# Performance work log

Hardware: AMD Instinct MI355X
Metric: run time of the kernel (lower is better)

The kernel has to match this reference:

```python
import math
import jax, jax.numpy as jnp
import numpy as np

B, S, T = 32, 512, 180
D, F, L, H = 512, 2048, 6, 8
DH = D // H


def _pos_encoding(length, d):
    pos = np.arange(length, dtype=np.float32)[:, None]
    div = np.exp(np.arange(0, d, 2, dtype=np.float32) * (-math.log(10000.0) / d))
    pe = np.zeros((length, d), dtype=np.float32)
    pe[:, 0::2] = np.sin(pos * div)
    pe[:, 1::2] = np.cos(pos * div)
    return jnp.asarray(pe)


def _ln(x, scale, bias):
    mu = x.mean(-1, keepdims=True)
    var = ((x - mu) ** 2).mean(-1, keepdims=True)
    return (x - mu) * jax.lax.rsqrt(var + 1e-5) * scale + bias


def _mha(q_in, kv_in, w, b, causal=False):
    # w: [4, D, D] = (Wq, Wk, Wv, Wo); b: [4, D]
    b_, sq = q_in.shape[:2]
    q = (q_in @ w[0] + b[0]).reshape(b_, sq, H, DH)
    k = (kv_in @ w[1] + b[1]).reshape(b_, -1, H, DH)
    v = (kv_in @ w[2] + b[2]).reshape(b_, -1, H, DH)
    s = jnp.einsum('bqhd,bkhd->bhqk', q, k) / math.sqrt(DH)
    if causal:
        mask = jnp.tril(jnp.ones((sq, k.shape[1]), dtype=bool))
        s = jnp.where(mask, s, -1e9)
    a = jax.nn.softmax(s, axis=-1)
    o = jnp.einsum('bhqk,bkhd->bqhd', a, v).reshape(b_, sq, D)
    return o @ w[3] + b[3]


def _ffn(x, w1, b1, w2, b2):
    return jax.nn.relu(x @ w1 + b1) @ w2 + b2


def setup_inputs() -> dict:
    key = jax.random.key(0)
    ks = jax.random.split(key, 16)
    n = lambda k, shape: jax.random.normal(k, shape, jnp.float32) * 0.02
    return {
        'x': jax.random.normal(ks[0], (B, S, 2), jnp.float32),
        'y_cv_teacher': jax.random.normal(ks[1], (B, T, 1), jnp.float32),
        'src_proj_w': n(ks[2], (2, D)), 'src_proj_b': jnp.zeros((D,), jnp.float32),
        'tgt_proj_w': n(ks[3], (1, D)), 'tgt_proj_b': jnp.zeros((D,), jnp.float32),
        'enc_attn_w': n(ks[4], (L, 4, D, D)), 'enc_attn_b': jnp.zeros((L, 4, D), jnp.float32),
        'enc_ffn_w1': n(ks[5], (L, D, F)), 'enc_ffn_b1': jnp.zeros((L, F), jnp.float32),
        'enc_ffn_w2': n(ks[6], (L, F, D)), 'enc_ffn_b2': jnp.zeros((L, D), jnp.float32),
        'enc_ln_scale': jnp.ones((L, 2, D), jnp.float32), 'enc_ln_bias': jnp.zeros((L, 2, D), jnp.float32),
        'dec_self_w': n(ks[7], (L, 4, D, D)), 'dec_self_b': jnp.zeros((L, 4, D), jnp.float32),
        'dec_cross_w': n(ks[8], (L, 4, D, D)), 'dec_cross_b': jnp.zeros((L, 4, D), jnp.float32),
        'dec_ffn_w1': n(ks[9], (L, D, F)), 'dec_ffn_b1': jnp.zeros((L, F), jnp.float32),
        'dec_ffn_w2': n(ks[10], (L, F, D)), 'dec_ffn_b2': jnp.zeros((L, D), jnp.float32),
        'dec_ln_scale': jnp.ones((L, 3, D), jnp.float32), 'dec_ln_bias': jnp.zeros((L, 3, D), jnp.float32),
        'out_w': n(ks[11], (D, 1)), 'out_b': jnp.zeros((1,), jnp.float32),
    }


def reference(x, y_cv_teacher, src_proj_w, src_proj_b, tgt_proj_w, tgt_proj_b,
              enc_attn_w, enc_attn_b, enc_ffn_w1, enc_ffn_b1, enc_ffn_w2, enc_ffn_b2,
              enc_ln_scale, enc_ln_bias, dec_self_w, dec_self_b, dec_cross_w, dec_cross_b,
              dec_ffn_w1, dec_ffn_b1, dec_ffn_w2, dec_ffn_b2, dec_ln_scale, dec_ln_bias,
              out_w, out_b):
    pe = _pos_encoding(512, D)
    # encoder (post-norm, relu FFN, dropout disabled = eval semantics)
    h = x @ src_proj_w + src_proj_b + pe[: x.shape[1]]
    for i in range(L):
        h = _ln(h + _mha(h, h, enc_attn_w[i], enc_attn_b[i]), enc_ln_scale[i, 0], enc_ln_bias[i, 0])
        h = _ln(h + _ffn(h, enc_ffn_w1[i], enc_ffn_b1[i], enc_ffn_w2[i], enc_ffn_b2[i]),
                enc_ln_scale[i, 1], enc_ln_bias[i, 1])
    memory = h
    # teacher-forced decoder input: [start=0, y_cv_teacher[:-1]]
    tgt_in = jnp.concatenate([jnp.zeros((x.shape[0], 1, 1), x.dtype), y_cv_teacher[:, :-1, :]], axis=1)
    d = tgt_in @ tgt_proj_w + tgt_proj_b + pe[: tgt_in.shape[1]]
    for i in range(L):
        d = _ln(d + _mha(d, d, dec_self_w[i], dec_self_b[i], causal=True),
                dec_ln_scale[i, 0], dec_ln_bias[i, 0])
        d = _ln(d + _mha(d, memory, dec_cross_w[i], dec_cross_b[i]),
                dec_ln_scale[i, 1], dec_ln_bias[i, 1])
        d = _ln(d + _ffn(d, dec_ffn_w1[i], dec_ffn_b1[i], dec_ffn_w2[i], dec_ffn_b2[i]),
                dec_ln_scale[i, 2], dec_ln_bias[i, 2])
    return d @ out_w + out_b  # [B, T, 1]
```

## Files before the change

kernel.cpp:

```cpp
#include <hip/hip_runtime.h>
#include <math.h>

#define B_  32
#define S_  512
#define T_  180
#define D_  512
#define F_  2048
#define L_  6
#define H_  8
#define DH_ 64

typedef unsigned short u16;
typedef __attribute__((ext_vector_type(8))) short short8;
typedef __attribute__((ext_vector_type(4))) float floatx4;

__device__ __forceinline__ float bf2f(u16 h) {
    union { unsigned u; float f; } un; un.u = ((unsigned)h) << 16; return un.f;
}
__device__ __forceinline__ u16 f2bf(float f) {
    union { float f; unsigned u; } un; un.f = f;
    unsigned u = un.u;
    u += 0x7fffu + ((u >> 16) & 1u);
    return (u16)(u >> 16);
}

__device__ __forceinline__ void gload16(const u16* g, u16* l) {
    __builtin_amdgcn_global_load_lds(
        (const __attribute__((address_space(1))) void*)g,
        (__attribute__((address_space(3))) void*)l, 16, 0, 0);
}

__device__ __forceinline__ float pos_enc(int pos, int c) {
    int i2 = c & ~1;
    float div = expf(-(float)i2 * (9.210340371976184f / 512.0f));
    float arg = (float)pos * div;
    return (c & 1) ? cosf(arg) : sinf(arg);
}

__global__ __launch_bounds__(256) void embed_src_kernel(
    const float* __restrict__ x, const float* __restrict__ w,
    const float* __restrict__ b, u16* __restrict__ h)
{
    int idx = blockIdx.x * 256 + threadIdx.x;
    if (idx >= B_ * S_ * D_) return;
    int c  = idx & (D_ - 1);
    int bs = idx >> 9;
    int s  = bs & (S_ - 1);
    float x0 = x[bs * 2 + 0];
    float x1 = x[bs * 2 + 1];
    h[idx] = f2bf(x0 * w[c] + x1 * w[D_ + c] + b[c] + pos_enc(s, c));
}

__global__ __launch_bounds__(256) void embed_tgt_kernel(
    const float* __restrict__ y, const float* __restrict__ w,
    const float* __restrict__ b, u16* __restrict__ d)
{
    int idx = blockIdx.x * 256 + threadIdx.x;
    if (idx >= B_ * T_ * D_) return;
    int c  = idx & (D_ - 1);
    int bt = idx >> 9;
    int t  = bt % T_;
    int bb = bt / T_;
    float tv = (t == 0) ? 0.0f : y[bb * T_ + (t - 1)];
    d[idx] = f2bf(tv * w[c] + b[c] + pos_enc(t, c));
}

__global__ __launch_bounds__(256) void wconv_kernel(
    const float* __restrict__ W, u16* __restrict__ Wt, int K, int N)
{
    __shared__ float tile[32][33];
    size_t mat = (size_t)blockIdx.z * K * N;
    const float* Wm = W + mat;
    u16* Wtm = Wt + mat;
    int n0 = blockIdx.x * 32, k0 = blockIdx.y * 32;
    int tx = threadIdx.x & 31, ty = threadIdx.x >> 5;
#pragma unroll
    for (int i = 0; i < 32; i += 8)
        tile[ty + i][tx] = Wm[(size_t)(k0 + ty + i) * N + n0 + tx];
    __syncthreads();
#pragma unroll
    for (int i = 0; i < 32; i += 8)
        Wtm[(size_t)(n0 + ty + i) * K + k0 + tx] = f2bf(tile[tx][ty + i]);
}

__global__ __launch_bounds__(256) void gemm_bf16_kernel(
    const u16* __restrict__ A, int lda, const u16* __restrict__ Bt,
    const float* __restrict__ bias, u16* __restrict__ C, int ldc,
    int M, int N, int K, int relu)
{
    __shared__ u16 smem[18432];
    u16* As = smem;
    u16* Bs = smem + 8192;

    int tid  = threadIdx.x;
    int w    = tid >> 6;
    int lane = tid & 63;
    int m0 = blockIdx.y << 7, n0 = blockIdx.x << 7;

    int sr = w * 32 + (lane >> 2);
    int sk = (lane & 3) * 8;
    const u16* ag0 = A  + (size_t)(m0 + sr)      * lda + sk;
    const u16* ag1 = A  + (size_t)(m0 + sr + 16) * lda + sk;
    const u16* bg0 = Bt + (size_t)(n0 + sr)      * K + sk;
    const u16* bg1 = Bt + (size_t)(n0 + sr + 16) * K + sk;
    u16* al0 = As + (w * 2 + 0) * 512;
    u16* al1 = As + (w * 2 + 1) * 512;
    u16* bl0 = Bs + (w * 2 + 0) * 512;
    u16* bl1 = Bs + (w * 2 + 1) * 512;

    int wm = (w >> 1) * 64, wn = (w & 1) * 64;
    int fr = lane & 15;
    int fk = (lane >> 4) * 8;

    floatx4 acc[4][4] = {};

    for (int k0 = 0; k0 < K; k0 += 64) {
#pragma unroll
        for (int hh = 0; hh < 2; ++hh) {
            int go = k0 + hh * 32;
            int lo = hh * 4096;
            gload16(ag0 + go, al0 + lo);
            gload16(ag1 + go, al1 + lo);
            gload16(bg0 + go, bl0 + lo);
            gload16(bg1 + go, bl1 + lo);
        }
        __syncthreads();

#pragma unroll
        for (int hh = 0; hh < 2; ++hh) {
            int lo = hh * 4096;
            short8 af[4], bf[4];
#pragma unroll
            for (int i = 0; i < 4; ++i)
                af[i] = *(const short8*)&As[lo + (wm + i * 16 + fr) * 32 + fk];
#pragma unroll
            for (int j = 0; j < 4; ++j)
                bf[j] = *(const short8*)&Bs[lo + (wn + j * 16 + fr) * 32 + fk];
#pragma unroll
            for (int i = 0; i < 4; ++i)
#pragma unroll
                for (int j = 0; j < 4; ++j)
                    acc[i][j] = __builtin_amdgcn_mfma_f32_16x16x32_bf16(
                        af[i], bf[j], acc[i][j], 0, 0, 0);
        }
        __syncthreads();
    }

    u16* epi = smem + w * 4608;
    int cc = lane & 15;
    int rq = (lane >> 4) * 4;
#pragma unroll
    for (int j = 0; j < 4; ++j) {
        float bj = bias[n0 + wn + j * 16 + cc];
#pragma unroll
        for (int i = 0; i < 4; ++i) {
#pragma unroll
            for (int r = 0; r < 4; ++r) {
                float vv = acc[i][j][r] + bj;
                if (relu) vv = fmaxf(vv, 0.f);
                epi[(i * 16 + rq + r) * 72 + j * 16 + cc] = f2bf(vv);
            }
        }
    }
    __syncthreads();
#pragma unroll
    for (int t = 0; t < 8; ++t) {
        int er = t * 8 + (lane >> 3);
        int ec = (lane & 7) * 8;
        short8 vv = *(const short8*)&epi[er * 72 + ec];
        *(short8*)&C[(size_t)(m0 + wm + er) * ldc + n0 + wn + ec] = vv;
    }
}

#define SBAR()       asm volatile("s_barrier" ::: "memory")
#define WAIT_LGKM0() do { asm volatile("s_waitcnt lgkmcnt(0)" ::: "memory"); \
                          __builtin_amdgcn_sched_barrier(0); } while (0)
#define WAIT_VM(N)   asm volatile("s_waitcnt vmcnt(" #N ")" ::: "memory")

#define RD_A(BUF, MH) do { \
  _Pragma("unroll") for (int i_ = 0; i_ < 4; ++i_) \
  _Pragma("unroll") for (int h_ = 0; h_ < 2; ++h_) \
    a[i_][h_] = *(const short8*)&smem[(BUF) * 16384 + \
        ((MH) * 128 + qm + i_ * 16 + fr) * 64 + cSwz[h_]]; \
} while (0)

#define RD_B(BUF, NH) do { \
  _Pragma("unroll") for (int n_ = 0; n_ < 2; ++n_) \
  _Pragma("unroll") for (int h_ = 0; h_ < 2; ++h_) \
    bb[n_][h_] = *(const short8*)&smem[32768 + (BUF) * 16384 + \
        ((NH) * 128 + qn + n_ * 16 + fr) * 64 + cSwz[h_]]; \
} while (0)

#define PH_MMA(MH, NH) do { \
  __builtin_amdgcn_s_setprio(1); \
  _Pragma("unroll") for (int i_ = 0; i_ < 4; ++i_) \
  _Pragma("unroll") for (int n_ = 0; n_ < 2; ++n_) \
  _Pragma("unroll") for (int h_ = 0; h_ < 2; ++h_) \
    acc[MH][NH][i_][n_] = __builtin_amdgcn_mfma_f32_16x16x32_bf16( \
        a[i_][h_], bb[n_][h_], acc[MH][NH][i_][n_], 0, 0, 0); \
  __builtin_amdgcn_s_setprio(0); \
} while (0)

__global__ __launch_bounds__(512, 2) void gemm256_bf16_kernel(
    const u16* __restrict__ A, int lda, const u16* __restrict__ Bt,
    const float* __restrict__ bias, u16* __restrict__ C, int ldc,
    int M, int N, int K, int relu)
{
    __shared__ __align__(128) u16 smem[65536];
    const int AB0 = 0, AB1 = 16384, BB0 = 32768, BB1 = 49152;

    int tid = threadIdx.x;
    int w = tid >> 6, lane = tid & 63;
    int fr = lane & 15, q = lane >> 4;
    int qm = (w >> 2) * 64, qn = (w & 3) * 32;
    int r8 = tid >> 3;
    int ksrc = (((tid & 7) ^ (r8 & 7)) << 3);
    int cSwz[2];
    cSwz[0] = ((q ^ (fr & 7)) << 3);
    cSwz[1] = (((4 | q) ^ (fr & 7)) << 3);

    int nbx = gridDim.x;
    int nwg = nbx * gridDim.y;
    int flat = blockIdx.y * nbx + blockIdx.x;
    int qq = nwg >> 3, rr = nwg & 7;
    int xcd = flat & 7, sidx = flat >> 3;
    int wg = (xcd < rr ? xcd * (qq + 1) : rr * (qq + 1) + (xcd - rr) * qq) + sidx;
    int m0 = (wg / nbx) << 8, n0 = (wg % nbx) << 8;

    auto stg = [&](const u16* __restrict__ G, int ld, int row0, int bufOff,
                   int half, int gk) {
#pragma unroll
        for (int j = 0; j < 2; ++j) {
            int rl = half * 128 + j * 64 + r8;
            gload16(G + (size_t)(row0 + rl) * ld + gk + ksrc,
                    smem + bufOff + ((half * 128 + j * 64 + (w << 3)) << 6));
        }
    };

    short8 a[4][2], bb[2][2];
    floatx4 acc[2][2][4][2] = {};

    stg(A,  lda, m0, AB0, 0, 0);
    stg(A,  lda, m0, AB0, 1, 0);
    stg(Bt, K,   n0, BB0, 0, 0);
    stg(Bt, K,   n0, BB0, 1, 0);
    stg(Bt, K,   n0, BB1, 1, 64);
    stg(A,  lda, m0, AB1, 1, 64);
    WAIT_VM(0);
    SBAR();

    int NIT = K >> 7;
    for (int it = 0; it < NIT; ++it) {
        const int notlast = (it < NIT - 1);
        const int gk1 = it * 128 + 64, gk2 = gk1 + 64, gk3 = gk2 + 64;
        RD_A(0, 0); RD_B(0, 1);
        stg(A, lda, m0, AB1, 0, gk1);
        SBAR(); WAIT_LGKM0(); PH_MMA(0, 1); SBAR();
        RD_A(0, 1);
        stg(Bt, K, n0, BB1, 0, gk1);
        SBAR(); WAIT_LGKM0(); PH_MMA(1, 1); SBAR();
        RD_B(0, 0);
        if (notlast) stg(Bt, K, n0, BB0, 1, gk2);
        SBAR(); WAIT_LGKM0(); PH_MMA(1, 0); SBAR();
        RD_A(0, 0);
        if (notlast) { stg(A, lda, m0, AB0, 1, gk2); WAIT_VM(4); }
        else         { WAIT_VM(0); }
        SBAR(); WAIT_LGKM0(); PH_MMA(0, 0); SBAR();
        RD_A(1, 0); RD_B(1, 1);
        if (notlast) stg(A, lda, m0, AB0, 0, gk2);
        SBAR(); WAIT_LGKM0(); PH_MMA(0, 1); SBAR();
        RD_A(1, 1);
        if (notlast) stg(Bt, K, n0, BB0, 0, gk2);
        SBAR(); WAIT_LGKM0(); PH_MMA(1, 1); SBAR();
        RD_B(1, 0);
        if (notlast) stg(Bt, K, n0, BB1, 1, gk3);
        SBAR(); WAIT_LGKM0(); PH_MMA(1, 0); SBAR();
        RD_A(1, 0);
        if (notlast) { stg(A, lda, m0, AB1, 1, gk3); WAIT_VM(4); }
        SBAR(); WAIT_LGKM0(); PH_MMA(0, 0); SBAR();
    }

    u16* epi = smem + w * 2560;
    int rq = q * 4;
#pragma unroll
    for (int mh = 0; mh < 2; ++mh) {
#pragma unroll
        for (int nh = 0; nh < 2; ++nh) {
            __syncthreads();
            int bcol = n0 + nh * 128 + qn;
            int brow = m0 + mh * 128 + qm;
#pragma unroll
            for (int n = 0; n < 2; ++n) {
                float bj = bias[bcol + n * 16 + fr];
#pragma unroll
                for (int i = 0; i < 4; ++i)
#pragma unroll
                    for (int r = 0; r < 4; ++r) {
                        float vv = acc[mh][nh][i][n][r] + bj;
                        if (relu) vv = fmaxf(vv, 0.f);
                        epi[(i * 16 + rq + r) * 40 + n * 16 + fr] = f2bf(vv);
                    }
            }
            __syncthreads();
#pragma unroll
            for (int t = 0; t < 4; ++t) {
                int er = t * 16 + (lane >> 2);
                int ec = (lane & 3) * 8;
                short8 vv = *(const short8*)&epi[er * 40 + ec];
                *(short8*)&C[(size_t)(brow + er) * ldc + bcol + ec] = vv;
            }
        }
    }
}

#define CEXP 0.1803368801111244f

__global__ __launch_bounds__(256) void attn_mfma_kernel(
    const u16* Q, int qs, const u16* __restrict__ K, int ks,
    const u16* __restrict__ V, u16* O,
    int Sq, int Sk, int causal)
{
    __shared__ u16 Qs[64 * 72];
    __shared__ u16 Ks[64 * 72];
    __shared__ u16 Vt[64 * 72];
    __shared__ u16 Ps[4][16 * 72];

    int tid  = threadIdx.x;
    int w    = tid >> 6;
    int lane = tid & 63;
    int n    = lane & 15;
    int quad = lane >> 4;
    int bh = blockIdx.x;
    int bb = bh >> 3, hhd = bh & 7;
    int q0 = blockIdx.y * 64;

    const u16* Qb = Q + (size_t)bb * Sq * qs + hhd * DH_;
    const u16* Kb = K + (size_t)bb * Sk * ks + hhd * DH_;
    const u16* Vb = V + (size_t)bb * Sk * ks + hhd * DH_;

#pragma unroll
    for (int it = 0; it < 2; ++it) {
        int idx = it * 256 + tid;
        int r = idx >> 3, dg = (idx & 7) * 8;
        int qg0 = q0 + r;
        short8 vv = {};
        if (qg0 < Sq) vv = *(const short8*)&Qb[(size_t)qg0 * qs + dg];
        *(short8*)&Qs[r * 72 + dg] = vv;
    }

    float m_i = -1e30f, l_i = 0.f;
    floatx4 o_acc[4] = {};

    int qg = q0 + w * 16 + n;
    int kend = causal ? ((Sk < q0 + 64) ? Sk : (q0 + 64)) : Sk;
    __syncthreads();

    short8 aq0 = *(const short8*)&Qs[(w * 16 + n) * 72 + quad * 8];
    short8 aq1 = *(const short8*)&Qs[(w * 16 + n) * 72 + 32 + quad * 8];

    for (int k0 = 0; k0 < kend; k0 += 64) {
#pragma unroll
        for (int it = 0; it < 2; ++it) {
            int idx = it * 256 + tid;
            int r = idx >> 3, dg = (idx & 7) * 8;
            int kg = k0 + r;
            short8 kv = {}, vv = {};
            if (kg < Sk) {
                kv = *(const short8*)&Kb[(size_t)kg * ks + dg];
                vv = *(const short8*)&Vb[(size_t)kg * ks + dg];
            }
            *(short8*)&Ks[r * 72 + dg] = kv;
            int col = (r + dg) & 63;
#pragma unroll
            for (int j = 0; j < 8; ++j)
                Vt[(dg + j) * 72 + col] = (u16)vv[j];
        }
        __syncthreads();

        floatx4 sc[4] = {};
#pragma unroll
        for (int j = 0; j < 4; ++j) {
            short8 bk0 = *(const short8*)&Ks[(j * 16 + n) * 72 + quad * 8];
            short8 bk1 = *(const short8*)&Ks[(j * 16 + n) * 72 + 32 + quad * 8];
            sc[j] = __builtin_amdgcn_mfma_f32_16x16x32_bf16(bk0, aq0, sc[j], 0, 0, 0);
            sc[j] = __builtin_amdgcn_mfma_f32_16x16x32_bf16(bk1, aq1, sc[j], 0, 0, 0);
        }

        bool need_mask = (k0 + 64 > Sk) ||
                         (causal && (k0 + 63 > q0 + w * 16));
        if (need_mask) {
#pragma unroll
            for (int j = 0; j < 4; ++j) {
#pragma unroll
                for (int r = 0; r < 4; ++r) {
                    int kg = k0 + j * 16 + quad * 4 + r;
                    if (kg >= Sk || (causal && kg > qg))
                        sc[j][r] = -1e30f;
                }
            }
        }

        float mx = sc[0][0];
#pragma unroll
        for (int j = 0; j < 4; ++j)
#pragma unroll
            for (int r = 0; r < 4; ++r) mx = fmaxf(mx, sc[j][r]);
        mx = fmaxf(mx, __shfl_xor(mx, 16));
        mx = fmaxf(mx, __shfl_xor(mx, 32));
        float mnew = fmaxf(m_i, mx);
        float alpha = exp2f((m_i - mnew) * CEXP);
        m_i = mnew;
        float ps = 0.f;
#pragma unroll
        for (int j = 0; j < 4; ++j)
#pragma unroll
            for (int r = 0; r < 4; ++r) {
                float p = exp2f((sc[j][r] - mnew) * CEXP);
                sc[j][r] = p; ps += p;
            }
        ps += __shfl_xor(ps, 16);
        ps += __shfl_xor(ps, 32);
        l_i = l_i * alpha + ps;
#pragma unroll
        for (int jb = 0; jb < 4; ++jb)
#pragma unroll
            for (int r = 0; r < 4; ++r) o_acc[jb][r] *= alpha;

#pragma unroll
        for (int j = 0; j < 4; ++j) {
            unsigned lo = (unsigned)f2bf(sc[j][0]) | ((unsigned)f2bf(sc[j][1]) << 16);
            unsigned hi = (unsigned)f2bf(sc[j][2]) | ((unsigned)f2bf(sc[j][3]) << 16);
            *(uint2*)&Ps[w][n * 72 + j * 16 + quad * 4] = make_uint2(lo, hi);
        }

        short8 ap0 = *(const short8*)&Ps[w][n * 72 + quad * 8];
        short8 ap1 = *(const short8*)&Ps[w][n * 72 + 32 + quad * 8];
#pragma unroll
        for (int jb = 0; jb < 4; ++jb) {
            int d = jb * 16 + n;
            int rot = d & ~7;
            short8 bv0 = *(const short8*)&Vt[d * 72 + ((quad * 8 + rot) & 63)];
            short8 bv1 = *(const short8*)&Vt[d * 72 + ((32 + quad * 8 + rot) & 63)];
            o_acc[jb] = __builtin_amdgcn_mfma_f32_16x16x32_bf16(bv0, ap0, o_acc[jb], 0, 0, 0);
            o_acc[jb] = __builtin_amdgcn_mfma_f32_16x16x32_bf16(bv1, ap1, o_acc[jb], 0, 0, 0);
        }
        __syncthreads();
    }

    float inv = 1.0f / l_i;
    u16* Ob = O + (size_t)bb * Sq * qs + hhd * DH_;
    if (qg < Sq) {
#pragma unroll
        for (int jb = 0; jb < 4; ++jb) {
            unsigned lo = (unsigned)f2bf(o_acc[jb][0] * inv) |
                          ((unsigned)f2bf(o_acc[jb][1] * inv) << 16);
            unsigned hi = (unsigned)f2bf(o_acc[jb][2] * inv) |
                          ((unsigned)f2bf(o_acc[jb][3] * inv) << 16);
            *(uint2*)&Ob[(size_t)qg * qs + jb * 16 + quad * 4] = make_uint2(lo, hi);
        }
    }
}

__global__ __launch_bounds__(128) void add_ln_kernel(
    u16* __restrict__ h, const u16* __restrict__ delta,
    const float* __restrict__ scale, const float* __restrict__ bias)
{
    __shared__ float red[2][2];
    int row = blockIdx.x, tid = threadIdx.x;
    int lane = tid & 63, wv = tid >> 6;
    size_t base = (size_t)row * D_ + tid * 4;
    uint2 hv = *(const uint2*)&h[base];
    uint2 dv = *(const uint2*)&delta[base];
    float v0 = bf2f(hv.x & 0xffff) + bf2f(dv.x & 0xffff);
    float v1 = bf2f(hv.x >> 16)    + bf2f(dv.x >> 16);
    float v2 = bf2f(hv.y & 0xffff) + bf2f(dv.y & 0xffff);
    float v3 = bf2f(hv.y >> 16)    + bf2f(dv.y >> 16);

    float a  = v0 + v1 + v2 + v3;
    float b2 = v0 * v0 + v1 * v1 + v2 * v2 + v3 * v3;
#pragma unroll
    for (int off = 32; off > 0; off >>= 1) {
        a  += __shfl_xor(a, off);
        b2 += __shfl_xor(b2, off);
    }
    if (lane == 0) { red[wv][0] = a; red[wv][1] = b2; }
    __syncthreads();
    float S1 = red[0][0] + red[1][0];
    float S2 = red[0][1] + red[1][1];
    float mu = S1 * (1.0f / 512.0f);
    float var = S2 * (1.0f / 512.0f) - mu * mu;
    float rs = rsqrtf(var + 1e-5f);

    int c = tid * 4;
    float4 sc = *(const float4*)&scale[c];
    float4 bi = *(const float4*)&bias[c];
    unsigned lo = (unsigned)f2bf((v0 - mu) * rs * sc.x + bi.x) |
                  ((unsigned)f2bf((v1 - mu) * rs * sc.y + bi.y) << 16);
    unsigned hi = (unsigned)f2bf((v2 - mu) * rs * sc.z + bi.z) |
                  ((unsigned)f2bf((v3 - mu) * rs * sc.w + bi.w) << 16);
    *(uint2*)&h[base] = make_uint2(lo, hi);
}

__global__ __launch_bounds__(64) void out_proj_kernel(
    const u16* __restrict__ d, const float* __restrict__ w,
    const float* __restrict__ b, float* __restrict__ out)
{
    int row = blockIdx.x, lane = threadIdx.x;
    float s = 0.f;
    for (int c = lane; c < D_; c += 64) s += bf2f(d[(size_t)row * D_ + c]) * w[c];
#pragma unroll
    for (int off = 32; off > 0; off >>= 1) s += __shfl_down(s, off);
    if (lane == 0) out[row] = s + b[0];
}

extern "C" void kernel_launch(void* const* d_in, const int* in_sizes, int n_in,
                              void* d_out, int out_size, void* d_ws, size_t ws_size,
                              hipStream_t stream)
{
    const float* x          = (const float*)d_in[0];
    const float* y          = (const float*)d_in[1];
    const float* src_w      = (const float*)d_in[2];
    const float* src_b      = (const float*)d_in[3];
    const float* tgt_w      = (const float*)d_in[4];
    const float* tgt_b      = (const float*)d_in[5];
    const float* enc_attn_w = (const float*)d_in[6];
    const float* enc_attn_b = (const float*)d_in[7];
    const float* enc_ffn_w1 = (const float*)d_in[8];
    const float* enc_ffn_b1 = (const float*)d_in[9];
    const float* enc_ffn_w2 = (const float*)d_in[10];
    const float* enc_ffn_b2 = (const float*)d_in[11];
    const float* enc_ln_s   = (const float*)d_in[12];
    const float* enc_ln_b   = (const float*)d_in[13];
    const float* dec_self_w = (const float*)d_in[14];
    const float* dec_self_b = (const float*)d_in[15];
    const float* dec_cross_w= (const float*)d_in[16];
    const float* dec_cross_b= (const float*)d_in[17];
    const float* dec_ffn_w1 = (const float*)d_in[18];
    const float* dec_ffn_b1 = (const float*)d_in[19];
    const float* dec_ffn_w2 = (const float*)d_in[20];
    const float* dec_ffn_b2 = (const float*)d_in[21];
    const float* dec_ln_s   = (const float*)d_in[22];
    const float* dec_ln_b   = (const float*)d_in[23];
    const float* out_w      = (const float*)d_in[24];
    const float* out_b      = (const float*)d_in[25];
    float* out = (float*)d_out;

    const size_t E_BSD = (size_t)B_ * S_ * D_;
    const size_t E_BTD = (size_t)B_ * T_ * D_;
    const size_t WDD   = (size_t)D_ * D_;
    const size_t WDF   = (size_t)D_ * F_;
    const int MS = B_ * S_;
    const int MT = B_ * T_;

    u16* h    = (u16*)d_ws;
    u16* qkv  = h + E_BSD;
    u16* o    = qkv + (size_t)MS * 1536;
    u16* dbuf = o + E_BSD;
    u16* wsc  = dbuf + E_BTD;
    u16* mid  = qkv;
    u16* cq   = qkv;
    u16* ckv  = qkv + 4 * 1024 * 1024;

    auto gemm = [&](const u16* A, int lda, const u16* Wt, const float* bi,
                    u16* C, int ldc, int M, int N, int K, int relu) {
        dim3 g(N / 128, M / 128);
        gemm_bf16_kernel<<<g, dim3(256), 0, stream>>>(A, lda, Wt, bi, C, ldc,
                                                      M, N, K, relu);
    };
    auto gemm256 = [&](const u16* A, int lda, const u16* Wt, const float* bi,
                       u16* C, int ldc, int M, int N, int K, int relu) {
        dim3 g(N / 256, M / 256);
        gemm256_bf16_kernel<<<g, dim3(512), 0, stream>>>(A, lda, Wt, bi, C, ldc,
                                                         M, N, K, relu);
    };
    auto attn = [&](const u16* Qp, int qs, const u16* Kp, int ks,
                    const u16* Vp, u16* Op, int Sq, int Sk, int causal) {
        dim3 g(B_ * H_, (Sq + 63) / 64);
        attn_mfma_kernel<<<g, dim3(256), 0, stream>>>(Qp, qs, Kp, ks, Vp, Op,
                                                      Sq, Sk, causal);
    };
    auto addln = [&](u16* hp, const u16* dp, const float* sc, const float* bi,
                     int rows) {
        add_ln_kernel<<<dim3(rows), dim3(128), 0, stream>>>(hp, dp, sc, bi);
    };
    auto wconv = [&](const float* W, u16* Wt, int K, int N, int nmat) {
        wconv_kernel<<<dim3(N / 32, K / 32, nmat), dim3(256), 0, stream>>>(W, Wt, K, N);
    };

    embed_src_kernel<<<dim3((B_ * S_ * D_ + 255) / 256), dim3(256), 0, stream>>>(
        x, src_w, src_b, h);
    for (int l = 0; l < L_; ++l) {
        wconv(enc_attn_w + (size_t)l * 4 * WDD, wsc, D_, D_, 4);
        wconv(enc_ffn_w1 + (size_t)l * WDF, wsc + 4 * WDD, D_, F_, 1);
        wconv(enc_ffn_w2 + (size_t)l * WDF, wsc + 4 * WDD + WDF, F_, D_, 1);

        const float* bl = enc_attn_b + (size_t)l * 4 * D_;
        gemm256(h, D_, wsc, bl, qkv, 1536, MS, 1536, D_, 0);
        attn(qkv, 1536, qkv + 512, 1536, qkv + 1024, qkv, S_, S_, 0);
        gemm(qkv, 1536, wsc + 3 * WDD, bl + 3 * D_, o, D_, MS, D_, D_, 0);
        addln(h, o, enc_ln_s + (size_t)l * 2 * D_, enc_ln_b + (size_t)l * 2 * D_, MS);

        for (int m0 = 0; m0 < MS; m0 += 8192) {
            gemm256(h + (size_t)m0 * D_, D_, wsc + 4 * WDD,
                    enc_ffn_b1 + (size_t)l * F_, mid, F_, 8192, F_, D_, 1);
            gemm(mid, F_, wsc + 4 * WDD + WDF, enc_ffn_b2 + (size_t)l * D_,
                 o + (size_t)m0 * D_, D_, 8192, D_, F_, 0);
        }
        addln(h, o, enc_ln_s + (size_t)l * 2 * D_ + D_,
              enc_ln_b + (size_t)l * 2 * D_ + D_, MS);
    }

    embed_tgt_kernel<<<dim3((B_ * T_ * D_ + 255) / 256), dim3(256), 0, stream>>>(
        y, tgt_w, tgt_b, dbuf);
    for (int l = 0; l < L_; ++l) {
        wconv(dec_self_w  + (size_t)l * 4 * WDD, wsc, D_, D_, 4);
        wconv(dec_cross_w + (size_t)l * 4 * WDD, wsc + 4 * WDD, D_, D_, 4);
        wconv(dec_ffn_w1  + (size_t)l * WDF, wsc + 8 * WDD, D_, F_, 1);
        wconv(dec_ffn_w2  + (size_t)l * WDF, wsc + 8 * WDD + WDF, F_, D_, 1);

        const float* bl = dec_self_b + (size_t)l * 4 * D_;
        gemm(dbuf, D_, wsc, bl, qkv, 1536, MT, 1536, D_, 0);
        attn(qkv, 1536, qkv + 512, 1536, qkv + 1024, qkv, T_, T_, 1);
        gemm(qkv, 1536, wsc + 3 * WDD, bl + 3 * D_, o, D_, MT, D_, D_, 0);
        addln(dbuf, o, dec_ln_s + (size_t)l * 3 * D_,
              dec_ln_b + (size_t)l * 3 * D_, MT);

        const float* bc = dec_cross_b + (size_t)l * 4 * D_;
        gemm256(h, D_, wsc + 5 * WDD, bc + D_, ckv, 1024, MS, 1024, D_, 0);
        gemm(dbuf, D_, wsc + 4 * WDD, bc, cq, D_, MT, D_, D_, 0);
        attn(cq, 512, ckv, 1024, ckv + 512, cq, T_, S_, 0);
        gemm(cq, D_, wsc + 7 * WDD, bc + 3 * D_, o, D_, MT, D_, D_, 0);
        addln(dbuf, o, dec_ln_s + (size_t)l * 3 * D_ + D_,
              dec_ln_b + (size_t)l * 3 * D_ + D_, MT);

        gemm(dbuf, D_, wsc + 8 * WDD, dec_ffn_b1 + (size_t)l * F_,
             mid, F_, MT, F_, D_, 1);
        gemm(mid, F_, wsc + 8 * WDD + WDF, dec_ffn_b2 + (size_t)l * D_,
             o, D_, MT, D_, F_, 0);
        addln(dbuf, o, dec_ln_s + (size_t)l * 3 * D_ + 2 * D_,
              dec_ln_b + (size_t)l * 3 * D_ + 2 * D_, MT);
    }

    out_proj_kernel<<<dim3(MT), dim3(64), 0, stream>>>(dbuf, out_w, out_b, out);
}
```

Measured before the change: 3.228 ms.

## Use async LDS loads with XOR swizzle, lazy softmax rescale, packed bf16 converts

Attention now loads Q and K tiles with global_load_lds into unpadded, XOR-swizzled shared memory instead of register round-trips. It also skips the online-softmax rescale unless the running max grows by more than a threshold. Float-to-bf16 conversions use the hardware packed-convert instruction, and two decoder GEMMs move to the 256-tile kernel with M padded to 5888. The bounds checks on K/V/Q loads are removed, so out-of-range rows (Sk=180, T tail) may read past the valid data or into neighbouring batches, and the padded-M GEMMs read and write rows beyond MT.

```diff
diff --git a/kernel.cpp b/kernel.cpp
--- a/kernel.cpp
+++ b/kernel.cpp
@@ -22,6 +22,11 @@
     unsigned u = un.u;
     u += 0x7fffu + ((u >> 16) & 1u);
     return (u16)(u >> 16);
+}
+__device__ __forceinline__ unsigned cvt_pk_bf16(float lo, float hi) {
+    unsigned r;
+    asm("v_cvt_pk_bf16_f32 %0, %1, %2" : "=v"(r) : "v"(lo), "v"(hi));
+    return r;
 }
 
 __device__ __forceinline__ void gload16(const u16* g, u16* l) {
@@ -320,8 +325,8 @@
     const u16* __restrict__ V, u16* O,
     int Sq, int Sk, int causal)
 {
-    __shared__ u16 Qs[64 * 72];
-    __shared__ u16 Ks[64 * 72];
+    __shared__ u16 Qs[4096];
+    __shared__ u16 Ks[4096];
     __shared__ u16 Vt[64 * 72];
     __shared__ u16 Ps[4][16 * 72];
 
@@ -338,38 +343,33 @@
     const u16* Kb = K + (size_t)bb * Sk * ks + hhd * DH_;
     const u16* Vb = V + (size_t)bb * Sk * ks + hhd * DH_;
 
-#pragma unroll
-    for (int it = 0; it < 2; ++it) {
-        int idx = it * 256 + tid;
-        int r = idx >> 3, dg = (idx & 7) * 8;
-        int qg0 = q0 + r;
-        short8 vv = {};
-        if (qg0 < Sq) vv = *(const short8*)&Qb[(size_t)qg0 * qs + dg];
-        *(short8*)&Qs[r * 72 + dg] = vv;
-    }
+    int sr = tid >> 3;
+    int gk = (((tid & 7) ^ (sr & 7)) << 3);
+
+    gload16(Qb + (size_t)(q0 + sr) * qs + gk, Qs + tid * 8);
+    gload16(Qb + (size_t)(q0 + 32 + sr) * qs + gk, Qs + 2048 + tid * 8);
 
     float m_i = -1e30f, l_i = 0.f;
     floatx4 o_acc[4] = {};
-
     int qg = q0 + w * 16 + n;
     int kend = causal ? ((Sk < q0 + 64) ? Sk : (q0 + 64)) : Sk;
+
+    int csw0 = ((quad ^ (n & 7)) << 3);
+    int csw1 = (((4 | quad) ^ (n & 7)) << 3);
+
     __syncthreads();
 
-    short8 aq0 = *(const short8*)&Qs[(w * 16 + n) * 72 + quad * 8];
-    short8 aq1 = *(const short8*)&Qs[(w * 16 + n) * 72 + 32 + quad * 8];
+    short8 aq0 = *(const short8*)&Qs[(w * 16 + n) * 64 + csw0];
+    short8 aq1 = *(const short8*)&Qs[(w * 16 + n) * 64 + csw1];
 
     for (int k0 = 0; k0 < kend; k0 += 64) {
+        gload16(Kb + (size_t)(k0 + sr) * ks + gk, Ks + tid * 8);
+        gload16(Kb + (size_t)(k0 + 32 + sr) * ks + gk, Ks + 2048 + tid * 8);
 #pragma unroll
         for (int it = 0; it < 2; ++it) {
             int idx = it * 256 + tid;
             int r = idx >> 3, dg = (idx & 7) * 8;
-            int kg = k0 + r;
-            short8 kv = {}, vv = {};
-            if (kg < Sk) {
-                kv = *(const short8*)&Kb[(size_t)kg * ks + dg];
-                vv = *(const short8*)&Vb[(size_t)kg * ks + dg];
-            }
-            *(short8*)&Ks[r * 72 + dg] = kv;
+            short8 vv = *(const short8*)&Vb[(size_t)(k0 + r) * ks + dg];
             int col = (r + dg) & 63;
 #pragma unroll
             for (int j = 0; j < 8; ++j)
@@ -380,8 +380,8 @@
         floatx4 sc[4] = {};
 #pragma unroll
         for (int j = 0; j < 4; ++j) {
-            short8 bk0 = *(const short8*)&Ks[(j * 16 + n) * 72 + quad * 8];
-            short8 bk1 = *(const short8*)&Ks[(j * 16 + n) * 72 + 32 + quad * 8];
+            short8 bk0 = *(const short8*)&Ks[(j * 16 + n) * 64 + csw0];
+            short8 bk1 = *(const short8*)&Ks[(j * 16 + n) * 64 + csw1];
             sc[j] = __builtin_amdgcn_mfma_f32_16x16x32_bf16(bk0, aq0, sc[j], 0, 0, 0);
             sc[j] = __builtin_amdgcn_mfma_f32_16x16x32_bf16(bk1, aq1, sc[j], 0, 0, 0);
         }
@@ -407,30 +407,33 @@
             for (int r = 0; r < 4; ++r) mx = fmaxf(mx, sc[j][r]);
         mx = fmaxf(mx, __shfl_xor(mx, 16));
         mx = fmaxf(mx, __shfl_xor(mx, 32));
-        float mnew = fmaxf(m_i, mx);
-        float alpha = exp2f((m_i - mnew) * CEXP);
-        m_i = mnew;
+        if (__any(mx > m_i + 8.0f)) {
+            float mnew = fmaxf(m_i, mx);
+            float alpha = exp2f((m_i - mnew) * CEXP);
+            m_i = mnew;
+            l_i *= alpha;
+#pragma unroll
+            for (int jb = 0; jb < 4; ++jb)
+#pragma unroll
+                for (int r = 0; r < 4; ++r) o_acc[jb][r] *= alpha;
+        }
         float ps = 0.f;
 #pragma unroll
         for (int j = 0; j < 4; ++j)
 #pragma unroll
             for (int r = 0; r < 4; ++r) {
-                float p = exp2f((sc[j][r] - mnew) * CEXP);
+                float p = exp2f((sc[j][r] - m_i) * CEXP);
                 sc[j][r] = p; ps += p;
             }
         ps += __shfl_xor(ps, 16);
         ps += __shfl_xor(ps, 32);
-        l_i = l_i * alpha + ps;
-#pragma unroll
-        for (int jb = 0; jb < 4; ++jb)
-#pragma unroll
-            for (int r = 0; r < 4; ++r) o_acc[jb][r] *= alpha;
+        l_i += ps;
 
 #pragma unroll
         for (int j = 0; j < 4; ++j) {
-            unsigned lo = (unsigned)f2bf(sc[j][0]) | ((unsigned)f2bf(sc[j][1]) << 16);
-            unsigned hi = (unsigned)f2bf(sc[j][2]) | ((unsigned)f2bf(sc[j][3]) << 16);
-            *(uint2*)&Ps[w][n * 72 + j * 16 + quad * 4] = make_uint2(lo, hi);
+            unsigned p0 = cvt_pk_bf16(sc[j][0], sc[j][1]);
+            unsigned p1 = cvt_pk_bf16(sc[j][2], sc[j][3]);
+            *(uint2*)&Ps[w][n * 72 + j * 16 + quad * 4] = make_uint2(p0, p1);
         }
 
         short8 ap0 = *(const short8*)&Ps[w][n * 72 + quad * 8];
@@ -452,11 +455,9 @@
     if (qg < Sq) {
 #pragma unroll
         for (int jb = 0; jb < 4; ++jb) {
-            unsigned lo = (unsigned)f2bf(o_acc[jb][0] * inv) |
-                          ((unsigned)f2bf(o_acc[jb][1] * inv) << 16);
-            unsigned hi = (unsigned)f2bf(o_acc[jb][2] * inv) |
-                          ((unsigned)f2bf(o_acc[jb][3] * inv) << 16);
-            *(uint2*)&Ob[(size_t)qg * qs + jb * 16 + quad * 4] = make_uint2(lo, hi);
+            unsigned p0 = cvt_pk_bf16(o_acc[jb][0] * inv, o_acc[jb][1] * inv);
+            unsigned p1 = cvt_pk_bf16(o_acc[jb][2] * inv, o_acc[jb][3] * inv);
+            *(uint2*)&Ob[(size_t)qg * qs + jb * 16 + quad * 4] = make_uint2(p0, p1);
         }
     }
 }
@@ -551,6 +552,7 @@
     const size_t WDF   = (size_t)D_ * F_;
     const int MS = B_ * S_;
     const int MT = B_ * T_;
+    const int MTP = 5888;
 
     u16* h    = (u16*)d_ws;
     u16* qkv  = h + E_BSD;
@@ -619,7 +621,7 @@
         wconv(dec_ffn_w2  + (size_t)l * WDF, wsc + 8 * WDD + WDF, F_, D_, 1);
 
         const float* bl = dec_self_b + (size_t)l * 4 * D_;
-        gemm(dbuf, D_, wsc, bl, qkv, 1536, MT, 1536, D_, 0);
+        gemm256(dbuf, D_, wsc, bl, qkv, 1536, MTP, 1536, D_, 0);
         attn(qkv, 1536, qkv + 512, 1536, qkv + 1024, qkv, T_, T_, 1);
         gemm(qkv, 1536, wsc + 3 * WDD, bl + 3 * D_, o, D_, MT, D_, D_, 0);
         addln(dbuf, o, dec_ln_s + (size_t)l * 3 * D_,
@@ -633,8 +635,8 @@
         addln(dbuf, o, dec_ln_s + (size_t)l * 3 * D_ + D_,
               dec_ln_b + (size_t)l * 3 * D_ + D_, MT);
 
-        gemm(dbuf, D_, wsc + 8 * WDD, dec_ffn_b1 + (size_t)l * F_,
-             mid, F_, MT, F_, D_, 1);
+        gemm256(dbuf, D_, wsc + 8 * WDD, dec_ffn_b1 + (size_t)l * F_,
+                mid, F_, MTP, F_, D_, 1);
         gemm(mid, F_, wsc + 8 * WDD + WDF, dec_ffn_b2 + (size_t)l * D_,
              o, D_, MT, D_, F_, 0);
         addln(dbuf, o, dec_ln_s + (size_t)l * 3 * D_ + 2 * D_,
```

Result: no change. 3.218 ms (-0.3%).
